# Performance work log

Hardware: AMD Instinct MI355X
Metric: run time of the kernel (lower is better)

Reference implementation:

```python
import jax, jax.numpy as jnp
import numpy as np

B, N, INC, H, W = 1, 6, 256, 56, 100
DD, CC = 41, 64                         # depth bins (4..45 step 1), cam feat channels
NX, NY, NZ = 33, 33, 2                  # BEV grid from pc_range=[-50,-50,-5,50,50,3], grid=3
CZ = CC * NZ                            # 128 channels into bevencode
DXV = jnp.array([3.0, 3.0, 3.0], jnp.float32)
BXV = jnp.array([-48.5, -48.5, -3.5], jnp.float32)


def _frustum():
    ds = jnp.arange(4.0, 45.0, 1.0)                      # (41,)
    xs = jnp.linspace(0.0, 1599.0, W)
    ys = jnp.linspace(0.0, 899.0, H)
    d = jnp.broadcast_to(ds[:, None, None], (DD, H, W))
    xg = jnp.broadcast_to(xs[None, None, :], (DD, H, W))
    yg = jnp.broadcast_to(ys[None, :, None], (DD, H, W))
    return jnp.stack([xg, yg, d], -1)                    # (D,H,W,3)


def _conv(x, w):
    return jax.lax.conv_general_dilated(x, w, (1, 1), 'SAME',
                                        dimension_numbers=('NCHW', 'OIHW', 'NCHW'))


def _bn_relu(x, s, b, m, v):
    inv = s / jnp.sqrt(v + 1e-5)
    return jax.nn.relu(x * inv[None, :, None, None] + (b - m * inv)[None, :, None, None])


def _forward(x, rots, trans, dn_w, dn_b,
             bw1, bn1_s, bn1_b, bn1_m, bn1_v,
             bw2, bn2_s, bn2_b, bn2_m, bn2_v,
             bw3, bn3_s, bn3_b, bn3_m, bn3_v,
             bw4, bn4_s, bn4_b, bn4_m, bn4_v):
    # ---- CamEncode: 1x1 depthnet -> softmax depth dist + context features ----
    xf = x.reshape(B * N, INC, H, W)
    y = _conv(xf, dn_w) + dn_b[None, :, None, None]
    depth = jax.nn.softmax(y[:, :DD], axis=1).reshape(B, N, DD, H, W)
    feat = y[:, DD:DD + CC].reshape(B, N, CC, H, W)
    # ---- get_geometry: (u*d, v*d, d) -> ego frame ----
    fr = _frustum()                                                     # (D,H,W,3)
    pts = jnp.concatenate([fr[..., :2] * fr[..., 2:3], fr[..., 2:3]], -1)
    geom = jnp.einsum('bnij,dhwj->bndhwi', rots, pts) + trans[:, :, None, None, None, :]
    # ---- voxel indices (torch .long() truncates toward zero) ----
    coor = ((geom - (BXV - DXV / 2.0)) / DXV).astype(jnp.int32)         # (B,N,D,H,W,3)
    cx, cy, cz = coor[..., 0], coor[..., 1], coor[..., 2]
    kept = (cx >= 0) & (cx < NX) & (cy >= 0) & (cy < NY) & (cz >= 0) & (cz < NZ)
    bidx = jnp.arange(B, dtype=jnp.int32)[:, None, None, None, None]
    ranks = ((bidx * NZ + cz) * NY + cy) * NX + cx                      # bev rank per point
    nvox = B * NZ * NY * NX
    seg = jnp.where(kept, ranks, nvox).reshape(-1)                      # drop bucket = nvox
    # ---- lift: depth-weighted outer product, splat: segment-sum by voxel ----
    vol = depth[..., None] * feat.transpose(0, 1, 3, 4, 2)[:, :, None]  # (B,N,D,H,W,C)
    bev = jax.ops.segment_sum(vol.reshape(-1, CC), seg, num_segments=nvox + 1)[:nvox]
    bev = bev.reshape(B, NZ, NY, NX, CC).transpose(0, 4, 1, 2, 3).reshape(B, CZ, NY, NX)
    h = _bn_relu(_conv(bev, bw1), bn1_s, bn1_b, bn1_m, bn1_v)
    h = _bn_relu(_conv(h, bw2), bn2_s, bn2_b, bn2_m, bn2_v)
    h = _bn_relu(_conv(h, bw3), bn3_s, bn3_b, bn3_m, bn3_v)
    h = _bn_relu(_conv(h, bw4), bn4_s, bn4_b, bn4_m, bn4_v)
    return h                                                            # (B,256,33,33)


def setup_inputs() -> dict:
    key = jax.random.key(0)
    ks = jax.random.split(key, 16)
    x = jax.random.normal(ks[0], (B, N, INC, H, W), jnp.float32)
    # rots = small rotation perturbation composed with intrinsics inverse
    kinv = jnp.array([[1.0 / 800.0, 0.0, -1.0], [0.0, 1.0 / 800.0, -0.5625], [0.0, 0.0, 1.0]], jnp.float32)
    R = jnp.eye(3, dtype=jnp.float32) + 0.05 * jax.random.normal(ks[1], (B, N, 3, 3), jnp.float32)
    rots = jnp.einsum('bnij,jk->bnik', R, kinv)
    trans = 2.0 * jax.random.normal(ks[2], (B, N, 3), jnp.float32)

    def w(k, o, i, kh, kw):
        return jax.random.normal(k, (o, i, kh, kw), jnp.float32) * (2.0 / (i * kh * kw)) ** 0.5

    def bn(k, c):
        k1, k2, k3, k4 = jax.random.split(k, 4)
        return (1.0 + 0.1 * jax.random.normal(k1, (c,), jnp.float32),
                0.1 * jax.random.normal(k2, (c,), jnp.float32),
                0.1 * jax.random.normal(k3, (c,), jnp.float32),
                jax.random.uniform(k4, (c,), jnp.float32, 0.5, 1.5))
    bn1 = bn(ks[7], CZ); bn2 = bn(ks[8], 512); bn3 = bn(ks[9], 512); bn4 = bn(ks[10], 256)
    return dict(
        x=x, rots=rots, trans=trans,
        dn_w=w(ks[3], DD + CC, INC, 1, 1), dn_b=jnp.zeros((DD + CC,), jnp.float32),
        bw1=w(ks[4], CZ, CZ, 3, 3),
        bn1_s=bn1[0], bn1_b=bn1[1], bn1_m=bn1[2], bn1_v=bn1[3],
        bw2=w(ks[5], 512, CZ, 3, 3),
        bn2_s=bn2[0], bn2_b=bn2[1], bn2_m=bn2[2], bn2_v=bn2[3],
        bw3=w(ks[6], 512, 512, 3, 3),
        bn3_s=bn3[0], bn3_b=bn3[1], bn3_m=bn3[2], bn3_v=bn3[3],
        bw4=w(ks[11], 256, 512, 3, 3),
        bn4_s=bn4[0], bn4_b=bn4[1], bn4_m=bn4[2], bn4_v=bn4[3])


def reference(x, rots, trans, dn_w, dn_b,
              bw1, bn1_s, bn1_b, bn1_m, bn1_v,
              bw2, bn2_s, bn2_b, bn2_m, bn2_v,
              bw3, bn3_s, bn3_b, bn3_m, bn3_v,
              bw4, bn4_s, bn4_b, bn4_m, bn4_v):
    return _forward(x, rots, trans, dn_w, dn_b,
                    bw1, bn1_s, bn1_b, bn1_m, bn1_v,
                    bw2, bn2_s, bn2_b, bn2_m, bn2_v,
                    bw3, bn3_s, bn3_b, bn3_m, bn3_v,
                    bw4, bn4_s, bn4_b, bn4_m, bn4_v)
```

## Files before the change

### kernel.cpp

```cpp
#include <hip/hip_runtime.h>
#include <math.h>

#define NCAM  6
#define INC   256
#define HH    56
#define WW    100
#define HW    5600
#define NPIX  33600
#define DDEP  41
#define CFEAT 64
#define NCH   105
#define NXG   33
#define NYG   33
#define NZG   2
#define NVOX  2178
#define PADW  35
#define PADHW 1225
#define NPIXO 1089

typedef short bf16x8 __attribute__((ext_vector_type(8)));
typedef float f32x4  __attribute__((ext_vector_type(4)));

#define Y_OFF    0
#define Y_SZ     (NCAM * NCH * HW)
#define WDH_OFF  (Y_OFF + Y_SZ)
#define WDL_OFF  (WDH_OFF + 16384)
#define W1H_OFF  (WDL_OFF + 16384)
#define W1L_OFF  (W1H_OFF + 73728)
#define W2H_OFF  (W1L_OFF + 73728)
#define W2L_OFF  (W2H_OFF + 294912)
#define W3H_OFF  (W2L_OFF + 294912)
#define W3L_OFF  (W3H_OFF + 1179648)
#define W4H_OFF  (W3L_OFF + 1179648)
#define W4L_OFF  (W4H_OFF + 589824)
#define BEV_OFF  (W4L_OFF + 589824)
#define BEV_SZ   (NVOX * CFEAT)
#define A0H_OFF  (BEV_OFF + BEV_SZ)
#define A0L_OFF  (A0H_OFF + 78400)
#define A1H_OFF  (A0L_OFF + 78400)
#define A1L_OFF  (A1H_OFF + 78400)
#define A2H_OFF  (A1L_OFF + 78400)
#define A2L_OFF  (A2H_OFF + 313600)
#define A3H_OFF  (A2L_OFF + 313600)
#define A3L_OFF  (A3H_OFF + 313600)
#define P_OFF    (A3L_OFF + 313600)
#define P_SZ     4460544
#define WS_END   (P_OFF + P_SZ)

__device__ __forceinline__ unsigned short f2bf_rn(float f) {
    unsigned u = __builtin_bit_cast(unsigned, f);
    unsigned r = (u + 0x7FFFu + ((u >> 16) & 1u)) >> 16;
    return (unsigned short)r;
}
__device__ __forceinline__ void split_bf(float f, unsigned short& h, unsigned short& l) {
    h = f2bf_rn(f);
    float hf = __builtin_bit_cast(float, (unsigned)h << 16);
    l = f2bf_rn(f - hf);
}

__device__ __forceinline__ void wprep_conv(const float* __restrict__ wgt,
                                           unsigned short* __restrict__ wh,
                                           unsigned short* __restrict__ wl,
                                           int COUT, int CIN, int i)
{
    int jj = i & 7, lane = (i >> 3) & 63;
    int r  = i >> 9;
    int nchk = CIN >> 5;
    int chk = r % nchk; r /= nchk;
    int ncog = COUT >> 4;
    int cog = r % ncog; int dydx = r / ncog;
    int co = cog * 16 + (lane & 15);
    int ci = chk * 32 + (lane >> 4) * 8 + jj;
    float w = wgt[((size_t)co * CIN + ci) * 9 + dydx];
    unsigned short h, l; split_bf(w, h, l);
    wh[i] = h; wl[i] = l;
}

__global__ __launch_bounds__(256) void k_wprep_all(const float* __restrict__ dnw,
                                                   const float* __restrict__ bw1,
                                                   const float* __restrict__ bw2,
                                                   const float* __restrict__ bw3,
                                                   const float* __restrict__ bw4,
                                                   unsigned short* __restrict__ wdh,
                                                   unsigned short* __restrict__ wdl,
                                                   unsigned short* __restrict__ w1h,
                                                   unsigned short* __restrict__ w1l,
                                                   unsigned short* __restrict__ w2h,
                                                   unsigned short* __restrict__ w2l,
                                                   unsigned short* __restrict__ w3h,
                                                   unsigned short* __restrict__ w3l,
                                                   unsigned short* __restrict__ w4h,
                                                   unsigned short* __restrict__ w4l)
{
    int i = blockIdx.x * 256 + threadIdx.x;
    if (i < 32768) {
        int jj = i & 7, lane = (i >> 3) & 63, chk = (i >> 9) & 7, ct = i >> 12;
        int co = ct * 16 + (lane & 15);
        int ci = chk * 32 + (lane >> 4) * 8 + jj;
        float w = (co < NCH) ? dnw[co * 256 + ci] : 0.f;
        unsigned short h, l; split_bf(w, h, l);
        wdh[i] = h; wdl[i] = l;
        return;
    }
    i -= 32768;
    if (i < 147456)  { wprep_conv(bw1, w1h, w1l, 128, 128, i); return; }
    i -= 147456;
    if (i < 589824)  { wprep_conv(bw2, w2h, w2l, 512, 128, i); return; }
    i -= 589824;
    if (i < 2359296) { wprep_conv(bw3, w3h, w3l, 512, 512, i); return; }
    i -= 2359296;
    if (i < 1179648) { wprep_conv(bw4, w4h, w4l, 256, 512, i); return; }
}

__global__ __launch_bounds__(256) void k_depthnet_fused(const float* __restrict__ x,
                                                        const unsigned short* __restrict__ wdh,
                                                        const unsigned short* __restrict__ wdl,
                                                        const float* __restrict__ dnb,
                                                        float* __restrict__ y)
{
    const int t  = threadIdx.x;
    const int w  = t >> 6;
    const int l  = t & 63;
    const int lp = l & 15;
    const int q  = l >> 4;
    const int n   = blockIdx.y;
    const int ct0 = blockIdx.z * 4;
    const int px  = blockIdx.x * 64 + w * 16 + lp;
    const bool pok = px < HW;
    const float* xl = x + (size_t)n * INC * HW + (pok ? px : 0);

    f32x4 acc[4];
#pragma unroll
    for (int ct = 0; ct < 4; ++ct) acc[ct] = (f32x4){0.f, 0.f, 0.f, 0.f};

#pragma unroll 2
    for (int ci0 = 0; ci0 < INC; ci0 += 32) {
        float bv[8];
#pragma unroll
        for (int jj = 0; jj < 8; ++jj)
            bv[jj] = xl[(size_t)(ci0 + q * 8 + jj) * HW];
        bf16x8 Bh, Bl;
#pragma unroll
        for (int jj = 0; jj < 8; ++jj) {
            unsigned short h, lo; split_bf(pok ? bv[jj] : 0.f, h, lo);
            Bh[jj] = (short)h; Bl[jj] = (short)lo;
        }
#pragma unroll
        for (int ct = 0; ct < 4; ++ct) {
            const size_t ab = (size_t)(((ct0 + ct) * 8 + (ci0 >> 5)) * 64 + l) * 8;
            bf16x8 Ah = *(const bf16x8*)&wdh[ab];
            bf16x8 Al = *(const bf16x8*)&wdl[ab];
            acc[ct] = __builtin_amdgcn_mfma_f32_16x16x32_bf16(Ah, Bh, acc[ct], 0, 0, 0);
            acc[ct] = __builtin_amdgcn_mfma_f32_16x16x32_bf16(Ah, Bl, acc[ct], 0, 0, 0);
            acc[ct] = __builtin_amdgcn_mfma_f32_16x16x32_bf16(Al, Bh, acc[ct], 0, 0, 0);
        }
    }

    float v[4][4];
#pragma unroll
    for (int ct = 0; ct < 4; ++ct)
#pragma unroll
        for (int j = 0; j < 4; ++j) {
            int co = (ct0 + ct) * 16 + q * 4 + j;
            v[ct][j] = acc[ct][j] + ((co < NCH) ? dnb[co] : 0.f);
        }

    if (ct0 == 0) {
        float m = -3.4e38f;
#pragma unroll
        for (int ct = 0; ct < 4; ++ct)
#pragma unroll
            for (int j = 0; j < 4; ++j) {
                int co = ct * 16 + q * 4 + j;
                if (co < DDEP) m = fmaxf(m, v[ct][j]);
            }
        m = fmaxf(m, __shfl_xor(m, 16));
        m = fmaxf(m, __shfl_xor(m, 32));
        float e[4][4];
        float s = 0.f;
#pragma unroll
        for (int ct = 0; ct < 4; ++ct)
#pragma unroll
            for (int j = 0; j < 4; ++j) {
                int co = ct * 16 + q * 4 + j;
                e[ct][j] = (co < DDEP) ? expf(v[ct][j] - m) : 0.f;
                s += e[ct][j];
            }
        s += __shfl_xor(s, 16);
        s += __shfl_xor(s, 32);
#pragma unroll
        for (int ct = 0; ct < 4; ++ct)
#pragma unroll
            for (int j = 0; j < 4; ++j) {
                int co = ct * 16 + q * 4 + j;
                if (co < DDEP) v[ct][j] = e[ct][j] / s;
            }
    }

    if (pok) {
#pragma unroll
        for (int ct = 0; ct < 4; ++ct)
#pragma unroll
            for (int j = 0; j < 4; ++j) {
                int co = (ct0 + ct) * 16 + q * 4 + j;
                if (co < NCH)
                    y[((size_t)n * NCH + co) * HW + px] = v[ct][j];
            }
    }
}

__global__ __launch_bounds__(256) void k_splat2(const float* __restrict__ y,
                                                const float* __restrict__ rots,
                                                const float* __restrict__ trans,
                                                float* __restrict__ bev)
{
    __shared__ int vox[32 * DDEP];
    const int t  = threadIdx.x;
    const int p0 = blockIdx.x * 32;

    for (int k = t; k < 32 * DDEP; k += 256) {
        int pl = k / DDEP, d = k - pl * DDEP;
        int p = p0 + pl;
        int vx = -1;
        {
            int n = p / HW, hw = p - n * HW;
            int wi = hw % WW, hi = hw / WW;
            const float su = 1599.0f / 99.0f;
            const float sv = 899.0f / 55.0f;
            float u = __fmul_rn((float)wi, su);
            float v = __fmul_rn((float)hi, sv);
            const float* r = rots + n * 9;
            const float* tr = trans + n * 3;
            float dd  = 4.0f + (float)d;
            float pxv = __fmul_rn(u, dd);
            float pyv = __fmul_rn(v, dd);
            float gx = __fadd_rn(__fadd_rn(__fadd_rn(__fmul_rn(r[0], pxv), __fmul_rn(r[1], pyv)), __fmul_rn(r[2], dd)), tr[0]);
            float gy = __fadd_rn(__fadd_rn(__fadd_rn(__fmul_rn(r[3], pxv), __fmul_rn(r[4], pyv)), __fmul_rn(r[5], dd)), tr[1]);
            float gz = __fadd_rn(__fadd_rn(__fadd_rn(__fmul_rn(r[6], pxv), __fmul_rn(r[7], pyv)), __fmul_rn(r[8], dd)), tr[2]);
            int cx = (int)__fdiv_rn(__fadd_rn(gx, 50.0f), 3.0f);
            int cy = (int)__fdiv_rn(__fadd_rn(gy, 50.0f), 3.0f);
            int cz = (int)__fdiv_rn(__fadd_rn(gz, 5.0f), 3.0f);
            if (cx >= 0 && cx < NXG && cy >= 0 && cy < NYG && cz >= 0 && cz < NZG)
                vx = (cz * NYG + cy) * NXG + cx;
        }
        vox[k] = vx;
    }
    __syncthreads();

    const int g  = t >> 5;
    const int pl = t & 31;
    const int p  = p0 + pl;
    int n = p / HW, hw = p - n * HW;
    const float* dbase = y + (size_t)n * NCH * HW + hw;
    const float* fbase = dbase + (size_t)DDEP * HW;
    float f[8];
#pragma unroll
    for (int j = 0; j < 8; ++j) f[j] = fbase[(size_t)(g * 8 + j) * HW];

    float a[8];
#pragma unroll
    for (int j = 0; j < 8; ++j) a[j] = 0.f;
    int cur = -1;
    for (int d = 0; d < DDEP; ++d) {
        int vx = vox[pl * DDEP + d];
        if (vx != cur) {
            if (cur >= 0) {
                float* vp = bev + (size_t)cur * CFEAT + g * 8;
#pragma unroll
                for (int j = 0; j < 8; ++j) atomicAdd(vp + j, a[j]);
            }
            cur = vx;
#pragma unroll
            for (int j = 0; j < 8; ++j) a[j] = 0.f;
        }
        if (vx >= 0) {
            float dval = dbase[(size_t)d * HW];
#pragma unroll
            for (int j = 0; j < 8; ++j) a[j] += __fmul_rn(dval, f[j]);
        }
    }
    if (cur >= 0) {
        float* vp = bev + (size_t)cur * CFEAT + g * 8;
#pragma unroll
        for (int j = 0; j < 8; ++j) atomicAdd(vp + j, a[j]);
    }
}

__global__ __launch_bounds__(256) void k_bev2act(const float* __restrict__ bev,
                                                 unsigned short* __restrict__ ah,
                                                 unsigned short* __restrict__ al)
{
    int i = blockIdx.x * 256 + threadIdx.x;
    if (i >= NVOX * CFEAT) return;
    int vx = i >> 6, c = i & 63;
    int cz = vx / NPIXO, rem = vx - cz * NPIXO;
    int yy = rem / NXG, xx = rem - yy * NXG;
    int ch = c * 2 + cz;
    int pos = (yy + 1) * PADW + xx + 1;
    unsigned short h, l; split_bf(bev[i], h, l);
    ah[pos * 128 + ch] = h;
    al[pos * 128 + ch] = l;
}

template<int CIN, int COUT, int SL>
__global__ __launch_bounds__(256) void k_conv_mfma(const unsigned short* __restrict__ ah,
                                                   const unsigned short* __restrict__ al,
                                                   const unsigned short* __restrict__ wh,
                                                   const unsigned short* __restrict__ wl,
                                                   float* __restrict__ P)
{
    constexpr int CI_PER = CIN / SL;
    constexpr int NCOB = COUT / 64;
    constexpr int G    = NCOB * SL;
    constexpr int GX   = G / 8;
    constexpr int POSN = 140;
    __shared__ unsigned short bs[POSN * 64];
    const int t  = threadIdx.x;
    const int w  = t >> 6;
    const int l  = t & 63;
    const int lp = l & 15;
    const int q  = l >> 4;

    const int bid   = blockIdx.x;
    const int xcd   = bid & 7;
    const int slot  = bid >> 3;
    const int ytile = slot % 17;
    const int gon   = slot / 17;
    const int group = xcd * GX + gon;
    const int cobi  = group % NCOB;
    const int sl    = group / NCOB;

    const int y0  = ytile * 2;
    const int cob = cobi * 64 + w * 16;
    const int ci_base = sl * CI_PER;

    int  pos0[5];
    bool vld[5];
#pragma unroll
    for (int ct = 0; ct < 5; ++ct) {
        int tp = ct * 16 + lp;
        int r = tp / 33, c = tp - r * 33;
        bool v = (tp < 66) && (y0 + r < 33);
        vld[ct]  = v;
        pos0[ct] = v ? (r * 35 + c) : 0;
    }

    f32x4 acc[5];
#pragma unroll
    for (int ct = 0; ct < 5; ++ct) acc[ct] = (f32x4){0.f, 0.f, 0.f, 0.f};

    for (int chk = 0; chk < CI_PER; chk += 32) {
        const int ci0 = ci_base + chk;
        __syncthreads();
        for (int i = t; i < POSN * 8; i += 256) {
            int pos = i >> 3, s = i & 7;
            int gpos = y0 * 35 + pos;
            const unsigned short* src = (s < 4) ? ah : al;
            int sp = s ^ (pos & 7);
            uint4 val = make_uint4(0u, 0u, 0u, 0u);
            if (gpos < PADHW)
                val = *(const uint4*)&src[(size_t)gpos * CIN + ci0 + (s & 3) * 8];
            *(uint4*)&bs[pos * 64 + sp * 8] = val;
        }
        __syncthreads();

#pragma unroll 3
        for (int dydx = 0; dydx < 9; ++dydx) {
            int dy = dydx / 3, dx = dydx - dy * 3;
            int off = dy * 35 + dx;
            const size_t abase = (size_t)(((dydx * (COUT >> 4) + (cob >> 4)) * (CIN >> 5)
                                           + (ci0 >> 5)) * 64 + l) * 8;
            bf16x8 Ah = *(const bf16x8*)&wh[abase];
            bf16x8 Al = *(const bf16x8*)&wl[abase];
#pragma unroll
            for (int ct = 0; ct < 5; ++ct) {
                int pos = pos0[ct] + off;
                int sph = q ^ (pos & 7);
                bf16x8 Bh = *(const bf16x8*)&bs[pos * 64 + sph * 8];
                bf16x8 Bl = *(const bf16x8*)&bs[pos * 64 + (sph ^ 4) * 8];
                acc[ct] = __builtin_amdgcn_mfma_f32_16x16x32_bf16(Ah, Bh, acc[ct], 0, 0, 0);
                acc[ct] = __builtin_amdgcn_mfma_f32_16x16x32_bf16(Ah, Bl, acc[ct], 0, 0, 0);
                acc[ct] = __builtin_amdgcn_mfma_f32_16x16x32_bf16(Al, Bh, acc[ct], 0, 0, 0);
            }
        }
    }

#pragma unroll
    for (int ct = 0; ct < 5; ++ct) {
        if (!vld[ct]) continue;
        int gp = y0 * 33 + ct * 16 + lp;
        float* dst = P + ((size_t)sl * NPIXO + gp) * COUT + cob + q * 4;
        *(f32x4*)dst = acc[ct];
    }
}

template<int SL>
__global__ __launch_bounds__(256) void k_finish(const float* __restrict__ P,
                                                const float* __restrict__ bns,
                                                const float* __restrict__ bnb,
                                                const float* __restrict__ bnm,
                                                const float* __restrict__ bnv,
                                                unsigned short* __restrict__ oh,
                                                unsigned short* __restrict__ ol,
                                                float* __restrict__ outf,
                                                int COUT)
{
    int i = blockIdx.x * 256 + threadIdx.x;
    if (i >= COUT * NPIXO) return;
    int co = i % COUT, p = i / COUT;
    float s = 0.f;
#pragma unroll
    for (int sl = 0; sl < SL; ++sl)
        s += P[((size_t)sl * NPIXO + p) * COUT + co];
    float sc = bns[co] / sqrtf(bnv[co] + 1e-5f);
    float bi = bnb[co] - bnm[co] * sc;
    float rv = fmaxf(fmaf(s, sc, bi), 0.f);
    if (outf) {
        outf[(size_t)co * NPIXO + p] = rv;
    } else {
        int yy = p / NXG, xx = p - yy * NXG;
        int pos = (yy + 1) * PADW + xx + 1;
        unsigned short h, lo; split_bf(rv, h, lo);
        oh[(size_t)pos * COUT + co] = h;
        ol[(size_t)pos * COUT + co] = lo;
    }
}

extern "C" void kernel_launch(void* const* d_in, const int* in_sizes, int n_in,
                              void* d_out, int out_size, void* d_ws, size_t ws_size,
                              hipStream_t stream)
{
    const float* x     = (const float*)d_in[0];
    const float* rots  = (const float*)d_in[1];
    const float* trans = (const float*)d_in[2];
    const float* dnw   = (const float*)d_in[3];
    const float* dnb   = (const float*)d_in[4];
    const float* bw1   = (const float*)d_in[5];
    const float* bn1s  = (const float*)d_in[6];
    const float* bn1b  = (const float*)d_in[7];
    const float* bn1m  = (const float*)d_in[8];
    const float* bn1v  = (const float*)d_in[9];
    const float* bw2   = (const float*)d_in[10];
    const float* bn2s  = (const float*)d_in[11];
    const float* bn2b  = (const float*)d_in[12];
    const float* bn2m  = (const float*)d_in[13];
    const float* bn2v  = (const float*)d_in[14];
    const float* bw3   = (const float*)d_in[15];
    const float* bn3s  = (const float*)d_in[16];
    const float* bn3b  = (const float*)d_in[17];
    const float* bn3m  = (const float*)d_in[18];
    const float* bn3v  = (const float*)d_in[19];
    const float* bw4   = (const float*)d_in[20];
    const float* bn4s  = (const float*)d_in[21];
    const float* bn4b  = (const float*)d_in[22];
    const float* bn4m  = (const float*)d_in[23];
    const float* bn4v  = (const float*)d_in[24];

    float* ws  = (float*)d_ws;
    float* y   = ws + Y_OFF;
    float* bev = ws + BEV_OFF;
    float* P   = ws + P_OFF;
    unsigned short* wdh = (unsigned short*)(ws + WDH_OFF);
    unsigned short* wdl = (unsigned short*)(ws + WDL_OFF);
    unsigned short* w1h = (unsigned short*)(ws + W1H_OFF);
    unsigned short* w1l = (unsigned short*)(ws + W1L_OFF);
    unsigned short* w2h = (unsigned short*)(ws + W2H_OFF);
    unsigned short* w2l = (unsigned short*)(ws + W2L_OFF);
    unsigned short* w3h = (unsigned short*)(ws + W3H_OFF);
    unsigned short* w3l = (unsigned short*)(ws + W3L_OFF);
    unsigned short* w4h = (unsigned short*)(ws + W4H_OFF);
    unsigned short* w4l = (unsigned short*)(ws + W4L_OFF);
    unsigned short* a0h = (unsigned short*)(ws + A0H_OFF);
    unsigned short* a0l = (unsigned short*)(ws + A0L_OFF);
    unsigned short* a1h = (unsigned short*)(ws + A1H_OFF);
    unsigned short* a1l = (unsigned short*)(ws + A1L_OFF);
    unsigned short* a2h = (unsigned short*)(ws + A2H_OFF);
    unsigned short* a2l = (unsigned short*)(ws + A2L_OFF);
    unsigned short* a3h = (unsigned short*)(ws + A3H_OFF);
    unsigned short* a3l = (unsigned short*)(ws + A3L_OFF);
    float* out = (float*)d_out;

    hipMemsetAsync(bev, 0, (size_t)(P_OFF - BEV_OFF) * sizeof(float), stream);

    k_wprep_all<<<16832, 256, 0, stream>>>(dnw, bw1, bw2, bw3, bw4,
                                           wdh, wdl, w1h, w1l, w2h, w2l,
                                           w3h, w3l, w4h, w4l);
    k_depthnet_fused<<<dim3(88, 6, 2), 256, 0, stream>>>(x, wdh, wdl, dnb, y);
    k_splat2<<<1050, 256, 0, stream>>>(y, rots, trans, bev);

    k_bev2act<<<(NVOX * CFEAT + 255) / 256, 256, 0, stream>>>(bev, a0h, a0l);

    k_conv_mfma<128, 128, 4><<<136, 256, 0, stream>>>(a0h, a0l, w1h, w1l, P);
    k_finish<4><<<(128 * NPIXO + 255) / 256, 256, 0, stream>>>(P, bn1s, bn1b, bn1m, bn1v, a1h, a1l, nullptr, 128);
    k_conv_mfma<128, 512, 4><<<544, 256, 0, stream>>>(a1h, a1l, w2h, w2l, P);
    k_finish<4><<<(512 * NPIXO + 255) / 256, 256, 0, stream>>>(P, bn2s, bn2b, bn2m, bn2v, a2h, a2l, nullptr, 512);
    k_conv_mfma<512, 512, 8><<<1088, 256, 0, stream>>>(a2h, a2l, w3h, w3l, P);
    k_finish<8><<<(512 * NPIXO + 255) / 256, 256, 0, stream>>>(P, bn3s, bn3b, bn3m, bn3v, a3h, a3l, nullptr, 512);
    k_conv_mfma<512, 256, 8><<<544, 256, 0, stream>>>(a3h, a3l, w4h, w4l, P);
    k_finish<8><<<(256 * NPIXO + 255) / 256, 256, 0, stream>>>(P, bn4s, bn4b, bn4m, bn4v, nullptr, nullptr, out, 256);
}
```

Before: 134.9 us.

## Merge depthnet channel halves into one block and stage all conv input chunks once

The depthnet kernel now computes all 7 output-channel tiles per block instead of splitting them across two z-blocks. This stops the input being loaded and converted twice, at the cost of more accumulator registers. The activation split into high and low bf16 parts now uses truncation instead of round-to-nearest, which is cheaper but may change the error of the hi/lo split. The conv kernel loads every input-channel chunk for its slice into shared memory in a single pass with one barrier, then runs the 3x3 taps over all chunks. This removes the per-chunk sync loop but increases LDS use, which may reduce occupancy.

```diff
diff --git a/kernel.cpp b/kernel.cpp
--- a/kernel.cpp
+++ b/kernel.cpp
@@ -57,6 +57,13 @@
     float hf = __builtin_bit_cast(float, (unsigned)h << 16);
     l = f2bf_rn(f - hf);
 }
+__device__ __forceinline__ void split_bf_trunc(float f, short& h, short& l) {
+    unsigned u = __builtin_bit_cast(unsigned, f);
+    h = (short)(u >> 16);
+    float hf = __builtin_bit_cast(float, u & 0xFFFF0000u);
+    float r = f - hf;
+    l = (short)(__builtin_bit_cast(unsigned, r) >> 16);
+}
 
 __device__ __forceinline__ void wprep_conv(const float* __restrict__ wgt,
                                            unsigned short* __restrict__ wh,
@@ -124,14 +131,13 @@
     const int lp = l & 15;
     const int q  = l >> 4;
     const int n   = blockIdx.y;
-    const int ct0 = blockIdx.z * 4;
     const int px  = blockIdx.x * 64 + w * 16 + lp;
     const bool pok = px < HW;
     const float* xl = x + (size_t)n * INC * HW + (pok ? px : 0);
 
-    f32x4 acc[4];
-#pragma unroll
-    for (int ct = 0; ct < 4; ++ct) acc[ct] = (f32x4){0.f, 0.f, 0.f, 0.f};
+    f32x4 acc[7];
+#pragma unroll
+    for (int ct = 0; ct < 7; ++ct) acc[ct] = (f32x4){0.f, 0.f, 0.f, 0.f};
 
 #pragma unroll 2
     for (int ci0 = 0; ci0 < INC; ci0 += 32) {
@@ -142,12 +148,12 @@
         bf16x8 Bh, Bl;
 #pragma unroll
         for (int jj = 0; jj < 8; ++jj) {
-            unsigned short h, lo; split_bf(pok ? bv[jj] : 0.f, h, lo);
-            Bh[jj] = (short)h; Bl[jj] = (short)lo;
-        }
-#pragma unroll
-        for (int ct = 0; ct < 4; ++ct) {
-            const size_t ab = (size_t)(((ct0 + ct) * 8 + (ci0 >> 5)) * 64 + l) * 8;
+            short h, lo; split_bf_trunc(pok ? bv[jj] : 0.f, h, lo);
+            Bh[jj] = h; Bl[jj] = lo;
+        }
+#pragma unroll
+        for (int ct = 0; ct < 7; ++ct) {
+            const size_t ab = (size_t)((ct * 8 + (ci0 >> 5)) * 64 + l) * 8;
             bf16x8 Ah = *(const bf16x8*)&wdh[ab];
             bf16x8 Al = *(const bf16x8*)&wdl[ab];
             acc[ct] = __builtin_amdgcn_mfma_f32_16x16x32_bf16(Ah, Bh, acc[ct], 0, 0, 0);
@@ -161,11 +167,11 @@
     for (int ct = 0; ct < 4; ++ct)
 #pragma unroll
         for (int j = 0; j < 4; ++j) {
-            int co = (ct0 + ct) * 16 + q * 4 + j;
-            v[ct][j] = acc[ct][j] + ((co < NCH) ? dnb[co] : 0.f);
-        }
-
-    if (ct0 == 0) {
+            int co = ct * 16 + q * 4 + j;
+            v[ct][j] = acc[ct][j] + dnb[co];
+        }
+
+    {
         float m = -3.4e38f;
 #pragma unroll
         for (int ct = 0; ct < 4; ++ct)
@@ -176,8 +182,8 @@
             }
         m = fmaxf(m, __shfl_xor(m, 16));
         m = fmaxf(m, __shfl_xor(m, 32));
+        float s = 0.f;
         float e[4][4];
-        float s = 0.f;
 #pragma unroll
         for (int ct = 0; ct < 4; ++ct)
 #pragma unroll
@@ -202,9 +208,16 @@
         for (int ct = 0; ct < 4; ++ct)
 #pragma unroll
             for (int j = 0; j < 4; ++j) {
-                int co = (ct0 + ct) * 16 + q * 4 + j;
+                int co = ct * 16 + q * 4 + j;
+                y[((size_t)n * NCH + co) * HW + px] = v[ct][j];
+            }
+#pragma unroll
+        for (int ct = 4; ct < 7; ++ct)
+#pragma unroll
+            for (int j = 0; j < 4; ++j) {
+                int co = ct * 16 + q * 4 + j;
                 if (co < NCH)
-                    y[((size_t)n * NCH + co) * HW + px] = v[ct][j];
+                    y[((size_t)n * NCH + co) * HW + px] = acc[ct][j] + dnb[co];
             }
     }
 }
@@ -310,11 +323,15 @@
                                                    float* __restrict__ P)
 {
     constexpr int CI_PER = CIN / SL;
+    constexpr int CHUNKS = CI_PER / 32;
+    constexpr int NSLOT  = CHUNKS * 8;
+    constexpr int SMASK  = NSLOT - 1;
+    constexpr int ROW    = CHUNKS * 64;
     constexpr int NCOB = COUT / 64;
     constexpr int G    = NCOB * SL;
     constexpr int GX   = G / 8;
     constexpr int POSN = 140;
-    __shared__ unsigned short bs[POSN * 64];
+    __shared__ unsigned short bs[POSN * ROW];
     const int t  = threadIdx.x;
     const int w  = t >> 6;
     const int l  = t & 63;
@@ -345,42 +362,48 @@
         pos0[ct] = v ? (r * 35 + c) : 0;
     }
 
+    for (int i = t; i < POSN * NSLOT; i += 256) {
+        int pos = i / NSLOT, s = i - pos * NSLOT;
+        int gpos = y0 * 35 + pos;
+        bool hi = s < CHUNKS * 4;
+        int sq = hi ? s : s - CHUNKS * 4;
+        int cio = (sq >> 2) * 32 + (sq & 3) * 8;
+        const unsigned short* src = hi ? ah : al;
+        int sp = s ^ (pos & SMASK);
+        uint4 val = make_uint4(0u, 0u, 0u, 0u);
+        if (gpos < PADHW)
+            val = *(const uint4*)&src[(size_t)gpos * CIN + ci_base + cio];
+        *(uint4*)&bs[pos * ROW + sp * 8] = val;
+    }
+    __syncthreads();
+
     f32x4 acc[5];
 #pragma unroll
     for (int ct = 0; ct < 5; ++ct) acc[ct] = (f32x4){0.f, 0.f, 0.f, 0.f};
 
-    for (int chk = 0; chk < CI_PER; chk += 32) {
-        const int ci0 = ci_base + chk;
-        __syncthreads();
-        for (int i = t; i < POSN * 8; i += 256) {
-            int pos = i >> 3, s = i & 7;
-            int gpos = y0 * 35 + pos;
-            const unsigned short* src = (s < 4) ? ah : al;
-            int sp = s ^ (pos & 7);
-            uint4 val = make_uint4(0u, 0u, 0u, 0u);
-            if (gpos < PADHW)
-                val = *(const uint4*)&src[(size_t)gpos * CIN + ci0 + (s & 3) * 8];
-            *(uint4*)&bs[pos * 64 + sp * 8] = val;
-        }
-        __syncthreads();
-
 #pragma unroll 3
-        for (int dydx = 0; dydx < 9; ++dydx) {
-            int dy = dydx / 3, dx = dydx - dy * 3;
-            int off = dy * 35 + dx;
+    for (int dydx = 0; dydx < 9; ++dydx) {
+        int dy = dydx / 3, dx = dydx - dy * 3;
+        int off = dy * 35 + dx;
+        bf16x8 Ah[CHUNKS], Al[CHUNKS];
+#pragma unroll
+        for (int c = 0; c < CHUNKS; ++c) {
             const size_t abase = (size_t)(((dydx * (COUT >> 4) + (cob >> 4)) * (CIN >> 5)
-                                           + (ci0 >> 5)) * 64 + l) * 8;
-            bf16x8 Ah = *(const bf16x8*)&wh[abase];
-            bf16x8 Al = *(const bf16x8*)&wl[abase];
-#pragma unroll
-            for (int ct = 0; ct < 5; ++ct) {
-                int pos = pos0[ct] + off;
-                int sph = q ^ (pos & 7);
-                bf16x8 Bh = *(const bf16x8*)&bs[pos * 64 + sph * 8];
-                bf16x8 Bl = *(const bf16x8*)&bs[pos * 64 + (sph ^ 4) * 8];
-                acc[ct] = __builtin_amdgcn_mfma_f32_16x16x32_bf16(Ah, Bh, acc[ct], 0, 0, 0);
-                acc[ct] = __builtin_amdgcn_mfma_f32_16x16x32_bf16(Ah, Bl, acc[ct], 0, 0, 0);
-                acc[ct] = __builtin_amdgcn_mfma_f32_16x16x32_bf16(Al, Bh, acc[ct], 0, 0, 0);
+                                           + (ci_base >> 5) + c) * 64 + l) * 8;
+            Ah[c] = *(const bf16x8*)&wh[abase];
+            Al[c] = *(const bf16x8*)&wl[abase];
+        }
+#pragma unroll
+        for (int ct = 0; ct < 5; ++ct) {
+            int pos = pos0[ct] + off;
+#pragma unroll
+            for (int c = 0; c < CHUNKS; ++c) {
+                int sph = (c * 4 + q) ^ (pos & SMASK);
+                bf16x8 Bh = *(const bf16x8*)&bs[pos * ROW + sph * 8];
+                bf16x8 Bl = *(const bf16x8*)&bs[pos * ROW + (sph ^ (CHUNKS * 4)) * 8];
+                acc[ct] = __builtin_amdgcn_mfma_f32_16x16x32_bf16(Ah[c], Bh, acc[ct], 0, 0, 0);
+                acc[ct] = __builtin_amdgcn_mfma_f32_16x16x32_bf16(Ah[c], Bl, acc[ct], 0, 0, 0);
+                acc[ct] = __builtin_amdgcn_mfma_f32_16x16x32_bf16(Al[c], Bh, acc[ct], 0, 0, 0);
             }
         }
     }
@@ -485,7 +508,7 @@
     k_wprep_all<<<16832, 256, 0, stream>>>(dnw, bw1, bw2, bw3, bw4,
                                            wdh, wdl, w1h, w1l, w2h, w2l,
                                            w3h, w3l, w4h, w4l);
-    k_depthnet_fused<<<dim3(88, 6, 2), 256, 0, stream>>>(x, wdh, wdl, dnb, y);
+    k_depthnet_fused<<<dim3(88, 6), 256, 0, stream>>>(x, wdh, wdl, dnb, y);
     k_splat2<<<1050, 256, 0, stream>>>(y, rots, trans, bev);
 
     k_bev2act<<<(NVOX * CFEAT + 255) / 256, 256, 0, stream>>>(bev, a0h, a0l);
```

Result: no change. 137.6 us (+2.0%).
